# Kernel optimization log

Measured on AMD Instinct MI355X. Metric: run time of the kernel, lower is better.

The kernel has to match this reference:

```python
import jax, jax.numpy as jnp
import numpy as np

# Faithful JAX port of torchvision rotate(img, -angle, BILINEAR) applied to every
# (image, angle) pair, matching torchvision's align_corners=False grid_sample math:
# for output pixel (yo, xo), with a = radians(angle) (sign of the module's -angle
# already folded in), centered coords X = xo-(W-1)/2, Y = yo-(H-1)/2:
#   src_x = cos(a)*X - sin(a)*Y + (W-1)/2
#   src_y = sin(a)*X + cos(a)*Y + (H-1)/2
# then bilinear sample with zero padding outside the image.

def rotate_batch(image_batch, angles):
    n, c, H, W = image_batch.shape  # c == 1 (required by original output assignment)
    img = image_batch[:, 0]         # (n, H, W)
    a = jnp.deg2rad(angles)         # (k,)
    cx = (W - 1) * 0.5
    cy = (H - 1) * 0.5
    X = (jnp.arange(W, dtype=image_batch.dtype) - cx)[None, None, :]  # (1,1,W)
    Y = (jnp.arange(H, dtype=image_batch.dtype) - cy)[None, :, None]  # (1,H,1)
    ca = jnp.cos(a)[:, None, None]  # (k,1,1)
    sa = jnp.sin(a)[:, None, None]
    sx = ca * X - sa * Y + cx       # (k,H,W) source x in pixel coords
    sy = sa * X + ca * Y + cy       # (k,H,W)

    x0f = jnp.floor(sx); y0f = jnp.floor(sy)
    wx = sx - x0f; wy = sy - y0f    # bilinear fractional weights
    x0 = x0f.astype(jnp.int32); y0 = y0f.astype(jnp.int32)
    x1 = x0 + 1; y1 = y0 + 1

    def gather(yi, xi):
        # zero-padding grid_sample: out-of-bounds corners contribute 0
        valid = (yi >= 0) & (yi < H) & (xi >= 0) & (xi < W)      # (k,H,W)
        yc = jnp.clip(yi, 0, H - 1)
        xc = jnp.clip(xi, 0, W - 1)
        vals = img[:, yc, xc]                                     # (n,k,H,W)
        return jnp.where(valid[None], vals, jnp.zeros((), image_batch.dtype))

    out = (gather(y0, x0) * ((1 - wy) * (1 - wx))[None]
         + gather(y0, x1) * ((1 - wy) * wx)[None]
         + gather(y1, x0) * (wy * (1 - wx))[None]
         + gather(y1, x1) * (wy * wx)[None])
    return out  # (n, k, H, W)


def setup_inputs() -> dict:
    key = jax.random.key(0)
    k_img, k_ang = jax.random.split(key)
    image_batch = jax.random.normal(k_img, (32, 1, 512, 512), dtype=jnp.float32)
    angles = jax.random.uniform(k_ang, (8,), dtype=jnp.float32) * 360.0  # degrees
    return {"image_batch": image_batch, "angles": angles}


def reference(image_batch, angles):
    return rotate_batch(image_batch, angles)
```

## Files before the change

kernel.cpp:

```cpp
#include <hip/hip_runtime.h>
#include <math.h>
#include <stdint.h>

#define N_IMG 32
#define N_ANG 8
#define H_ 512
#define W_ 512

#define TX 64
#define TY 32
#define LP 84
#define NCHUNK 25
#define LWORDS (NCHUNK * 256)

__global__ __launch_bounds__(256, 5) void rotate_tile_kernel(
    const float* __restrict__ img,
    const float* __restrict__ angles,
    float* __restrict__ out)
{
    __shared__ float tile[LWORDS];

    const int bz   = blockIdx.z;
    const int k    = bz >> 1;
    const int n0   = (bz & 1) * (N_IMG / 2);
    const int tx0  = blockIdx.x * TX;
    const int ty0  = blockIdx.y * TY;
    const int tid  = threadIdx.x;
    const int wid  = tid >> 6;
    const int lane = tid & 63;

    const float rad = angles[k] * 0.017453292519943295f;
    float sa, ca;
    sincosf(rad, &sa, &ca);
    const float cx = (W_ - 1) * 0.5f;
    const float cy = (H_ - 1) * 0.5f;

    float minsx = 1e30f, maxsx = -1e30f, minsy = 1e30f, maxsy = -1e30f;
#pragma unroll
    for (int cyi = 0; cyi < 2; ++cyi) {
#pragma unroll
        for (int cxi = 0; cxi < 2; ++cxi) {
            const float xr = (float)(tx0 + cxi * (TX - 1)) - cx;
            const float yr = (float)(ty0 + cyi * (TY - 1)) - cy;
            const float sx = ca * xr - sa * yr + cx;
            const float sy = sa * xr + ca * yr + cy;
            minsx = fminf(minsx, sx); maxsx = fmaxf(maxsx, sx);
            minsy = fminf(minsy, sy); maxsy = fmaxf(maxsy, sy);
        }
    }
    const int bx0 = min(max((int)floorf(minsx) - 1, 0), W_ - 1);
    const int by0 = min(max((int)floorf(minsy) - 1, 0), H_ - 1);
    const int bx0m = (bx0 & ~3) - 4;
    const int by0m = by0 - 1;

    int goff[7];
    int nst = 0;
    for (int s = wid; s < NCHUNK; s += 4) {
        const int f   = s * 256 + lane * 4;
        const int row = f / LP;
        const int col = f - row * LP;
        const int grow = min(max(by0m + row, 0), H_ - 1);
        const int gcol = min(max(bx0m + col, 0), W_ - 4);
        goff[nst++] = grow * W_ + gcol;
    }

    const bool modeA = fabsf(ca) >= fabsf(sa);
    const int pxg = modeA ? (tid & 15) : (tid >> 4);
    const int py0 = modeA ? (tid >> 4) : (tid & 15);
    const int px  = pxg * 4;

    int   ob[2][4];
    float w00[2][4], w01[2][4], w10[2][4], w11[2][4];
#pragma unroll
    for (int p = 0; p < 2; ++p) {
        const int   yy = ty0 + py0 + p * 16;
        const float yr = (float)yy - cy;
#pragma unroll
        for (int j = 0; j < 4; ++j) {
            const int   xx = tx0 + px + j;
            const float xr = (float)xx - cx;
            const float sxs = ca * xr - sa * yr + cx;
            const float sys = sa * xr + ca * yr + cy;
            const float x0f = floorf(sxs), y0f = floorf(sys);
            const float wx = sxs - x0f, wy = sys - y0f;
            const int x0 = (int)x0f, y0 = (int)y0f;
            const bool vx0 = ((unsigned)x0       < (unsigned)W_);
            const bool vx1 = ((unsigned)(x0 + 1) < (unsigned)W_);
            const bool vy0 = ((unsigned)y0       < (unsigned)H_);
            const bool vy1 = ((unsigned)(y0 + 1) < (unsigned)H_);
            const int lx = min(max(x0 - bx0m, 0), 82);
            const int ly = min(max(y0 - by0m, 0), 74);
            ob[p][j] = ly * LP + lx;
            const float omwx = 1.0f - wx, omwy = 1.0f - wy;
            w00[p][j] = omwy * omwx * (float)(vy0 && vx0);
            w01[p][j] = omwy * wx   * (float)(vy0 && vx1);
            w10[p][j] = wy   * omwx * (float)(vy1 && vx0);
            w11[p][j] = wy   * wx   * (float)(vy1 && vx1);
        }
    }

    for (int n = n0; n < n0 + N_IMG / 2; ++n) {
        const float* __restrict__ ib = img + (size_t)n * (H_ * W_);
        for (int i = 0; i < nst; ++i) {
            __builtin_amdgcn_global_load_lds(
                (const __attribute__((address_space(1))) void*)(ib + goff[i]),
                (__attribute__((address_space(3))) void*)(&tile[(wid + i * 4) * 256]),
                16, 0, 0);
        }
        __syncthreads();

        float* __restrict__ outn =
            out + ((size_t)(n * N_ANG + k) * H_ + ty0) * W_ + tx0;
#pragma unroll
        for (int p = 0; p < 2; ++p) {
            float v[4];
#pragma unroll
            for (int j = 0; j < 4; ++j) {
                const float* __restrict__ b0 = &tile[ob[p][j]];
                v[j] = w00[p][j] * b0[0]
                     + w01[p][j] * b0[1]
                     + w10[p][j] * b0[LP]
                     + w11[p][j] * b0[LP + 1];
            }
            float4* dst = (float4*)(outn + (py0 + p * 16) * W_ + px);
            *dst = make_float4(v[0], v[1], v[2], v[3]);
        }
        __syncthreads();
    }
}

extern "C" void kernel_launch(void* const* d_in, const int* in_sizes, int n_in,
                              void* d_out, int out_size, void* d_ws, size_t ws_size,
                              hipStream_t stream) {
    const float* img    = (const float*)d_in[0];
    const float* angles = (const float*)d_in[1];
    float* out          = (float*)d_out;

    dim3 block(256, 1, 1);
    dim3 grid(W_ / TX, H_ / TY, N_ANG * 2);
    rotate_tile_kernel<<<grid, block, 0, stream>>>(img, angles, out);
}
```

Baseline: 353.2 us.

## Double-buffer LDS image tiles and shrink tile width to prefetch next image

```diff
diff --git a/kernel.cpp b/kernel.cpp
--- a/kernel.cpp
+++ b/kernel.cpp
@@ -7,18 +7,18 @@
 #define H_ 512
 #define W_ 512
 
-#define TX 64
+#define TX 32
 #define TY 32
-#define LP 84
-#define NCHUNK 25
+#define LP 56
+#define NCHUNK 11
 #define LWORDS (NCHUNK * 256)
 
-__global__ __launch_bounds__(256, 5) void rotate_tile_kernel(
+__global__ __launch_bounds__(256) void rotate_tile_kernel(
     const float* __restrict__ img,
     const float* __restrict__ angles,
     float* __restrict__ out)
 {
-    __shared__ float tile[LWORDS];
+    __shared__ float tile[2][LWORDS];
 
     const int bz   = blockIdx.z;
     const int k    = bz >> 1;
@@ -53,7 +53,7 @@
     const int bx0m = (bx0 & ~3) - 4;
     const int by0m = by0 - 1;
 
-    int goff[7];
+    int goff[3];
     int nst = 0;
     for (int s = wid; s < NCHUNK; s += 4) {
         const int f   = s * 256 + lane * 4;
@@ -65,15 +65,14 @@
     }
 
     const bool modeA = fabsf(ca) >= fabsf(sa);
-    const int pxg = modeA ? (tid & 15) : (tid >> 4);
-    const int py0 = modeA ? (tid >> 4) : (tid & 15);
+    const int pxg = modeA ? (tid & 7) : (tid >> 5);
+    const int py  = modeA ? (tid >> 3) : (tid & 31);
     const int px  = pxg * 4;
 
-    int   ob[2][4];
-    float w00[2][4], w01[2][4], w10[2][4], w11[2][4];
-#pragma unroll
-    for (int p = 0; p < 2; ++p) {
-        const int   yy = ty0 + py0 + p * 16;
+    int   ob[4];
+    float w00[4], w01[4], w10[4], w11[4];
+    {
+        const int   yy = ty0 + py;
         const float yr = (float)yy - cy;
 #pragma unroll
         for (int j = 0; j < 4; ++j) {
@@ -88,44 +87,53 @@
             const bool vx1 = ((unsigned)(x0 + 1) < (unsigned)W_);
             const bool vy0 = ((unsigned)y0       < (unsigned)H_);
             const bool vy1 = ((unsigned)(y0 + 1) < (unsigned)H_);
-            const int lx = min(max(x0 - bx0m, 0), 82);
-            const int ly = min(max(y0 - by0m, 0), 74);
-            ob[p][j] = ly * LP + lx;
+            const int lx = min(max(x0 - bx0m, 0), 54);
+            const int ly = min(max(y0 - by0m, 0), 47);
+            ob[j] = ly * LP + lx;
             const float omwx = 1.0f - wx, omwy = 1.0f - wy;
-            w00[p][j] = omwy * omwx * (float)(vy0 && vx0);
-            w01[p][j] = omwy * wx   * (float)(vy0 && vx1);
-            w10[p][j] = wy   * omwx * (float)(vy1 && vx0);
-            w11[p][j] = wy   * wx   * (float)(vy1 && vx1);
+            w00[j] = omwy * omwx * (float)(vy0 && vx0);
+            w01[j] = omwy * wx   * (float)(vy0 && vx1);
+            w10[j] = wy   * omwx * (float)(vy1 && vx0);
+            w11[j] = wy   * wx   * (float)(vy1 && vx1);
         }
     }
 
-    for (int n = n0; n < n0 + N_IMG / 2; ++n) {
-        const float* __restrict__ ib = img + (size_t)n * (H_ * W_);
-        for (int i = 0; i < nst; ++i) {
+    {
+        const float* __restrict__ ib = img + (size_t)n0 * (H_ * W_);
+        for (int i = 0; i < nst; ++i)
             __builtin_amdgcn_global_load_lds(
                 (const __attribute__((address_space(1))) void*)(ib + goff[i]),
-                (__attribute__((address_space(3))) void*)(&tile[(wid + i * 4) * 256]),
+                (__attribute__((address_space(3))) void*)(&tile[0][(wid + i * 4) * 256]),
                 16, 0, 0);
-        }
+    }
+
+    for (int i = 0; i < N_IMG / 2; ++i) {
+        const int n = n0 + i;
         __syncthreads();
 
-        float* __restrict__ outn =
-            out + ((size_t)(n * N_ANG + k) * H_ + ty0) * W_ + tx0;
+        if (i + 1 < N_IMG / 2) {
+            const float* __restrict__ ibn = img + (size_t)(n + 1) * (H_ * W_);
+            float* dstbuf = tile[(i + 1) & 1];
+            for (int s = 0; s < nst; ++s)
+                __builtin_amdgcn_global_load_lds(
+                    (const __attribute__((address_space(1))) void*)(ibn + goff[s]),
+                    (__attribute__((address_space(3))) void*)(&dstbuf[(wid + s * 4) * 256]),
+                    16, 0, 0);
+        }
+
+        const float* __restrict__ buf = tile[i & 1];
+        float v[4];
 #pragma unroll
-        for (int p = 0; p < 2; ++p) {
-            float v[4];
-#pragma unroll
-            for (int j = 0; j < 4; ++j) {
-                const float* __restrict__ b0 = &tile[ob[p][j]];
-                v[j] = w00[p][j] * b0[0]
-                     + w01[p][j] * b0[1]
-                     + w10[p][j] * b0[LP]
-                     + w11[p][j] * b0[LP + 1];
-            }
-            float4* dst = (float4*)(outn + (py0 + p * 16) * W_ + px);
-            *dst = make_float4(v[0], v[1], v[2], v[3]);
+        for (int j = 0; j < 4; ++j) {
+            const float* __restrict__ b0 = &buf[ob[j]];
+            v[j] = w00[j] * b0[0]
+                 + w01[j] * b0[1]
+                 + w10[j] * b0[LP]
+                 + w11[j] * b0[LP + 1];
         }
-        __syncthreads();
+        float4* dst = (float4*)(out + ((size_t)(n * N_ANG + k) * H_ + ty0 + py) * W_
+                                + tx0 + px);
+        *dst = make_float4(v[0], v[1], v[2], v[3]);
     }
 }
 
```

Result: slower. 374.8 us (+6.1%).
